# Optimization experiments

Measured on AMD Instinct MI355X. Metric: run time of the kernel, lower is better.

The kernel has to match this reference:

```python
import jax, jax.numpy as jnp
import numpy as np

A_MAX = 1.63
D_X = 0.0
E_STAR = 0.032
S_IMM = 0.14
S_INFTY = 0.049
X_H_STAR = 97.3
X_NU_STAR = 4.8
X_P_STAR = 1514.4
X_Y_STAR = 3.5
ALPHA_M = 0.9
ALPHA_M_STAR = 2.53
DELTA = 5
GAMMA_P = 2.04
NU = 4.8  # is_Garki = True
SIGMA_0 = 0.66 ** 0.5
SIGMA_I = 10.2 ** 0.5
N = 32768   # individuals
T = 365     # timesteps (max_age = T*DELTA = 1825 days)
M = 65536   # fixed infection pool (replaces dynamic tau_infidx list)


def _body_surface(age_days):
    age = jnp.minimum(age_days, 20.0 * 365.0) / 365.0
    b = 2.009715297378839e-1
    c = 1.7984405384216584e-1
    d = -2.121587990857579e-2
    e = 1.3554013908681017e-3
    f = -2.847697353524861e-5
    return b + c * age + d * age ** 2 + e * age ** 3 + f * age ** 4


def setup_inputs() -> dict:
    key = jax.random.key(0)
    k0, k1, k2, k3, k4, k5, k6 = jax.random.split(key, 7)
    EIR = jax.random.uniform(k0, (365 // DELTA,), minval=0.0, maxval=2.0)
    log_d = SIGMA_I * jax.random.normal(k1, (N,))  # log of LogNormal(0, sigma_i)
    offsets = jnp.sort(jax.random.randint(k2, (N,), 0, T * DELTA)).astype(jnp.int32)
    tau0 = jnp.floor(jax.random.uniform(k3, (M,)) * T) * DELTA          # infection start (days)
    tau_max = tau0 + jnp.exp(5.13 + 0.8 * jax.random.normal(k4, (M,)))  # infection end
    idx = jax.random.randint(k5, (M,), 0, N).astype(jnp.int32)           # host individual
    eps = jax.random.normal(k6, (T, M))                                  # parasite-density noise
    return dict(EIR=EIR, log_d=log_d, tau0=tau0, tau_max=tau_max, eps=eps,
                idx=idx, offsets=offsets)


def reference(EIR, log_d, tau0, tau_max, eps, idx, offsets):
    n = log_d.shape[0]
    Tn, Mn = eps.shape
    t_days = jnp.arange(Tn) * DELTA
    tf = t_days.astype(jnp.float32)
    eff_EIR = EIR[(t_days % 365) // DELTA] * _body_surface(tf) / A_MAX   # [T]
    D_m_t = 1.0 - ALPHA_M * jnp.exp(-(tf / 365.0 / ALPHA_M_STAR) * jnp.log(2.0))  # [T]

    # _ln_y_G time-independent pieces (per infection)
    dur = tau_max - tau0
    a = jnp.minimum(0.018 * dur, 4.4)
    c = a / (1.0 + dur / 35.0)
    b = jnp.log(a / c) / dur
    log_d_inf = log_d[idx]

    def step(carry, inp):
        X_p, X_h, X_y, _ = carry
        t_step, eps_t = inp
        t_int = t_step * DELTA
        t = t_int.astype(jnp.float32)
        act = t_int >= offsets                                  # [n] alive mask
        rel_idx = jnp.clip((t_int - offsets) // DELTA, 0, Tn - 1)
        E = jnp.where(act, eff_EIR[rel_idx], 0.0)               # [n]
        # _force_of_infection (Poisson replaced by its mean for determinism)
        S1 = S_INFTY + (1.0 - S_INFTY) / (1.0 + E / E_STAR)
        S2 = S_IMM + (1.0 - S_IMM) / (1.0 + (X_p / X_P_STAR) ** GAMMA_P)
        h_star = S1 * S2 * E
        # active infections this step
        m = (tau0 <= t) & (tau_max > t) & act[idx]              # [M]
        mf = m.astype(E.dtype)
        # _update_immunity (state BEFORE X_h update, as in original)
        sigma_y = SIGMA_0 * (1.0 + X_h / X_NU_STAR) ** -0.5     # [n]
        D_h = 1.0 / (1.0 + X_h / X_H_STAR)                      # [n]
        D_y = 1.0 / (1.0 + X_y / X_Y_STAR)                      # [M]
        Dm_i = D_m_t[rel_idx]                                   # [n]
        cnt = jax.ops.segment_sum(mf, idx, num_segments=n)      # multiplicity M
        M_inf = cnt[idx]
        ln_yG = a * jnp.exp(-b * (t - tau0)) - NU
        ln_yG = jnp.where(ln_yG <= 0.0, 1e-10, ln_yG)
        log_term = jnp.log(D_X / jnp.maximum(M_inf, 1.0) + (1.0 - D_X))
        E_ln_y = D_y * D_h[idx] * Dm_i[idx] * (log_d_inf + ln_yG) + log_term
        y = jnp.exp(E_ln_y + sigma_y[idx] * eps_t) * mf          # [M]
        Y = jax.ops.segment_sum(y, idx, num_segments=n)          # [n] total density
        X_p_new = X_p + E
        X_h_new = X_h + h_star
        X_y_new = X_y + (Y[idx] - y) * mf                        # cross-immunity
        return (X_p_new, X_h_new, X_y_new, Y), None

    init = (jnp.zeros(n), jnp.zeros(n), jnp.zeros(Mn), jnp.zeros(n))
    (X_p, X_h, X_y, Y), _ = jax.lax.scan(step, init, (jnp.arange(Tn), eps))
    return Y, X_y, X_h
```

## Files before the change

### kernel.cpp

```cpp
#include <hip/hip_runtime.h>

#define NHOST 32768
#define MINF  65536
#define TSTEPS 365
#define DELTA_ 5
#define KMAX  3
#define NGRP  4096
#define NWAVE 2048

#define C_E_STAR      0.032f
#define C_S_IMM       0.14f
#define C_S_INFTY     0.049f
#define C_X_H_STAR    97.3f
#define C_X_NU_STAR   4.8f
#define C_X_P_STAR    1514.4f
#define C_X_Y_STAR    3.5f
#define C_ALPHA_M     0.9f
#define C_ALPHA_M_ST  2.53f
#define C_GAMMA_P     2.04f
#define C_SIGMA_0     0.8124038404635961f
#define C_LN2         0.6931471805599453f


__global__ void initK(int* __restrict__ cnt, int* __restrict__ cursor) {
    int i = blockIdx.x * blockDim.x + threadIdx.x;
    if (i < NHOST) { cnt[i] = 0; cursor[i] = 0; }
}

__global__ void histK(const int* __restrict__ idx, int* __restrict__ cnt) {
    int j = blockIdx.x * blockDim.x + threadIdx.x;
    if (j < MINF) atomicAdd(&cnt[idx[j]], 1);
}

__global__ __launch_bounds__(1024) void scanK(const int* __restrict__ cnt,
                                              int* __restrict__ start) {
    __shared__ int sh[1024];
    int tid = threadIdx.x;
    int base = tid * 32;
    int s = 0;
    #pragma unroll
    for (int k = 0; k < 32; ++k) s += cnt[base + k];
    sh[tid] = s;
    __syncthreads();
    for (int o = 1; o < 1024; o <<= 1) {
        int v = 0;
        if (tid >= o) v = sh[tid - o];
        __syncthreads();
        sh[tid] += v;
        __syncthreads();
    }
    int run = sh[tid] - s;
    #pragma unroll
    for (int k = 0; k < 32; ++k) {
        start[base + k] = run;
        run += cnt[base + k];
    }
}

__global__ void scatterK(const int* __restrict__ idx,
                         const float* __restrict__ tau0,
                         const float* __restrict__ tau_max,
                         const int* __restrict__ start,
                         int* __restrict__ cursor,
                         int* __restrict__ slotJ,
                         float* __restrict__ slotT0,
                         float* __restrict__ slotT1) {
    int j = blockIdx.x * blockDim.x + threadIdx.x;
    if (j >= MINF) return;
    int h = idx[j];
    int p = start[h] + atomicAdd(&cursor[h], 1);
    slotJ[p]  = j;
    slotT0[p] = tau0[j];
    slotT1[p] = tau_max[j];
}

__global__ __launch_bounds__(512) void tableK(const float* __restrict__ EIR,
                                              float* __restrict__ sigyT,
                                              float* __restrict__ coefT,
                                              float* __restrict__ XhP) {
    __shared__ float sA[512];
    int r = threadIdx.x;
    float E = 0.0f, Dm = 0.0f;
    if (r < TSTEPS) {
        float tf  = (float)(r * DELTA_);
        float age = fminf(tf, 7300.0f) * (1.0f / 365.0f);
        float bs  = 2.009715297378839e-1f +
                    age * (1.7984405384216584e-1f +
                    age * (-2.121587990857579e-2f +
                    age * (1.3554013908681017e-3f +
                    age * (-2.847697353524861e-5f))));
        E  = EIR[r % 73] * bs * (1.0f / 1.63f);
        Dm = 1.0f - C_ALPHA_M * expf(-(tf / 365.0f / C_ALPHA_M_ST) * C_LN2);
    }
    sA[r] = E;
    __syncthreads();
    for (int o = 1; o < 512; o <<= 1) {
        float v = 0.0f;
        if (r >= o) v = sA[r - o];
        __syncthreads();
        sA[r] += v;
        __syncthreads();
    }
    float Xp = (r < TSTEPS) ? (sA[r] - E) : 0.0f;
    float S1    = C_S_INFTY + (1.0f - C_S_INFTY) / (1.0f + E * (1.0f / C_E_STAR));
    float p204  = __powf(Xp * (1.0f / C_X_P_STAR), C_GAMMA_P);
    float S2    = C_S_IMM + (1.0f - C_S_IMM) / (1.0f + p204);
    float hstar = S1 * S2 * E;
    __syncthreads();
    sA[r] = hstar;
    __syncthreads();
    for (int o = 1; o < 512; o <<= 1) {
        float v = 0.0f;
        if (r >= o) v = sA[r - o];
        __syncthreads();
        sA[r] += v;
        __syncthreads();
    }
    if (r < TSTEPS) {
        float Xh = sA[r] - hstar;
        sigyT[r] = C_SIGMA_0 * rsqrtf(1.0f + Xh * (1.0f / C_X_NU_STAR));
        coefT[r] = Dm / (1.0f + Xh * (1.0f / C_X_H_STAR));
        XhP[r]   = sA[r];
    }
}


__global__ __launch_bounds__(256) void mainK(const float* __restrict__ log_d,
                                             const int* __restrict__ offsets,
                                             const float* __restrict__ eps,
                                             const int* __restrict__ start,
                                             const int* __restrict__ cnt,
                                             const int* __restrict__ slotJ,
                                             const float* __restrict__ slotT0,
                                             const float* __restrict__ slotT1,
                                             const float* __restrict__ sigyTg,
                                             const float* __restrict__ coefTg,
                                             const float* __restrict__ XhPg,
                                             float* __restrict__ out) {
    __shared__ float sSig[TSTEPS];
    __shared__ float sCoef[TSTEPS];
    for (int k = threadIdx.x; k < TSTEPS; k += blockDim.x) {
        sSig[k]  = sigyTg[k];
        sCoef[k] = coefTg[k];
    }
    __syncthreads();

    int w    = blockIdx.x * 4 + (threadIdx.x >> 6);
    int lane = threadIdx.x & 63;
    int sub  = lane & 7;
    int hoff = lane >> 3;

    #pragma unroll 1
    for (int ph = 0; ph < 2; ++ph) {
        int g = ph ? (NGRP - 1 - w) : w;
        int h = g * 8 + hoff;

        int off = offsets[h];
        int ch  = cnt[h];
        int myCnt = (ch > sub) ? ((ch - sub + 7) >> 3) : 0;
        if (myCnt > KMAX) myCnt = KMAX;
        int base = start[h] + sub;
        float ld = log_d[h] + 1e-10f;

        int   J[KMAX];
        float T0[KMAX], T1[KMAX], Xy[KMAX], ec[KMAX];
        #pragma unroll
        for (int k = 0; k < KMAX; ++k) {
            Xy[k] = 0.0f; ec[k] = 0.0f; J[k] = 0;
            T0[k] = 1e30f; T1[k] = -1e30f;
            if (k < myCnt) {
                int p = base + 8 * k;
                J[k]  = slotJ[p];
                T0[k] = slotT0[p];
                T1[k] = slotT1[p];
            }
        }

        int tstart = (off + DELTA_ - 1) / DELTA_;
        float Ylast = 0.0f;

        if (tstart < TSTEPS) {
            float tf0 = (float)(tstart * DELTA_);
            #pragma unroll
            for (int k = 0; k < KMAX; ++k)
                if (T0[k] <= tf0 && T1[k] > tf0)
                    ec[k] = eps[(size_t)tstart * MINF + J[k]];
        }

        for (int t = tstart; t < TSTEPS; ++t) {
            float tf  = (float)(t * DELTA_);
            int   rel = t - tstart;

            float en[KMAX];
            #pragma unroll
            for (int k = 0; k < KMAX; ++k) en[k] = 0.0f;
            if (t < TSTEPS - 1) {
                float tf2 = tf + (float)DELTA_;
                #pragma unroll
                for (int k = 0; k < KMAX; ++k)
                    if (T0[k] <= tf2 && T1[k] > tf2)
                        en[k] = eps[(size_t)(t + 1) * MINF + J[k]];
            }

            float sigy = sSig[rel];
            float coef = sCoef[rel];

            float ysum = 0.0f;
            float yk[KMAX];
            bool  ak[KMAX];
            #pragma unroll
            for (int k = 0; k < KMAX; ++k) {
                bool  act = (T0[k] <= tf) & (T1[k] > tf);
                float Dy  = 1.0f / (1.0f + Xy[k] * (1.0f / C_X_Y_STAR));
                float y   = act ? __expf(Dy * coef * ld + sigy * ec[k]) : 0.0f;
                ak[k] = act; yk[k] = y; ysum += y;
            }
            float Ys = ysum + __shfl_xor(ysum, 1, 64);
            Ys += __shfl_xor(Ys, 2, 64);
            Ys += __shfl_xor(Ys, 4, 64);

            #pragma unroll
            for (int k = 0; k < KMAX; ++k)
                if (ak[k]) Xy[k] += Ys - yk[k];

            Ylast = Ys;

            #pragma unroll
            for (int k = 0; k < KMAX; ++k) ec[k] = en[k];
        }

        int iters = TSTEPS - tstart;
        if (sub == 0) {
            out[h] = Ylast;
            out[NHOST + MINF + h] = (iters > 0) ? XhPg[iters - 1] : 0.0f;
        }
        #pragma unroll
        for (int k = 0; k < KMAX; ++k)
            if (k < myCnt) out[NHOST + J[k]] = Xy[k];
    }
}


extern "C" void kernel_launch(void* const* d_in, const int* in_sizes, int n_in,
                              void* d_out, int out_size, void* d_ws, size_t ws_size,
                              hipStream_t stream) {
    const float* EIR     = (const float*)d_in[0];
    const float* log_d   = (const float*)d_in[1];
    const float* tau0    = (const float*)d_in[2];
    const float* tau_max = (const float*)d_in[3];
    const float* eps     = (const float*)d_in[4];
    const int*   idx     = (const int*)d_in[5];
    const int*   offsets = (const int*)d_in[6];
    float* out = (float*)d_out;

    char* ws = (char*)d_ws;
    int*   cnt    = (int*)ws;    ws += NHOST * sizeof(int);
    int*   start  = (int*)ws;    ws += NHOST * sizeof(int);
    int*   cursor = (int*)ws;    ws += NHOST * sizeof(int);
    int*   slotJ  = (int*)ws;    ws += MINF * sizeof(int);
    float* slotT0 = (float*)ws;  ws += MINF * sizeof(float);
    float* slotT1 = (float*)ws;  ws += MINF * sizeof(float);
    float* sigyT  = (float*)ws;  ws += TSTEPS * sizeof(float);
    float* coefT  = (float*)ws;  ws += TSTEPS * sizeof(float);
    float* XhP    = (float*)ws;  ws += TSTEPS * sizeof(float);

    initK<<<NHOST / 256, 256, 0, stream>>>(cnt, cursor);
    histK<<<MINF / 256, 256, 0, stream>>>(idx, cnt);
    scanK<<<1, 1024, 0, stream>>>(cnt, start);
    scatterK<<<MINF / 256, 256, 0, stream>>>(idx, tau0, tau_max, start, cursor,
                                             slotJ, slotT0, slotT1);
    tableK<<<1, 512, 0, stream>>>(EIR, sigyT, coefT, XhP);
    mainK<<<(NWAVE * 64) / 256, 256, 0, stream>>>(log_d, offsets, eps,
                                                  start, cnt, slotJ, slotT0, slotT1,
                                                  sigyT, coefT, XhP, out);
}
```

Baseline: 387.6 us.

## Map four lanes per host and prefetch eps two steps ahead

Each host's infections are now split across 4 lanes instead of 8, and each lane holds up to 6 infections instead of 3. The two-phase load-balancing loop over wave groups is dropped in favour of one thread group per host. The eps noise loads are software-pipelined two timesteps ahead, and the per-step table values are prefetched one step ahead. The aim is to hide global-memory latency on the dependent time loop and use fewer shuffle stages, at the cost of more registers per thread and possible imbalance between waves because offsets are sorted.

Measured after the change: 363.8 us. -6.1%, faster.

```diff
diff --git a/kernel.cpp b/kernel.cpp
--- a/kernel.cpp
+++ b/kernel.cpp
@@ -4,9 +4,7 @@
 #define MINF  65536
 #define TSTEPS 365
 #define DELTA_ 5
-#define KMAX  3
-#define NGRP  4096
-#define NWAVE 2048
+#define KMAX  6
 
 #define C_E_STAR      0.032f
 #define C_S_IMM       0.14f
@@ -137,107 +135,110 @@
                                              const float* __restrict__ coefTg,
                                              const float* __restrict__ XhPg,
                                              float* __restrict__ out) {
-    __shared__ float sSig[TSTEPS];
-    __shared__ float sCoef[TSTEPS];
+    __shared__ float sSig[TSTEPS + 1];
+    __shared__ float sCoef[TSTEPS + 1];
     for (int k = threadIdx.x; k < TSTEPS; k += blockDim.x) {
         sSig[k]  = sigyTg[k];
         sCoef[k] = coefTg[k];
     }
-    __syncthreads();
-
-    int w    = blockIdx.x * 4 + (threadIdx.x >> 6);
-    int lane = threadIdx.x & 63;
-    int sub  = lane & 7;
-    int hoff = lane >> 3;
-
-    #pragma unroll 1
-    for (int ph = 0; ph < 2; ++ph) {
-        int g = ph ? (NGRP - 1 - w) : w;
-        int h = g * 8 + hoff;
-
-        int off = offsets[h];
-        int ch  = cnt[h];
-        int myCnt = (ch > sub) ? ((ch - sub + 7) >> 3) : 0;
-        if (myCnt > KMAX) myCnt = KMAX;
-        int base = start[h] + sub;
-        float ld = log_d[h] + 1e-10f;
-
-        int   J[KMAX];
-        float T0[KMAX], T1[KMAX], Xy[KMAX], ec[KMAX];
-        #pragma unroll
-        for (int k = 0; k < KMAX; ++k) {
-            Xy[k] = 0.0f; ec[k] = 0.0f; J[k] = 0;
-            T0[k] = 1e30f; T1[k] = -1e30f;
-            if (k < myCnt) {
-                int p = base + 8 * k;
-                J[k]  = slotJ[p];
-                T0[k] = slotT0[p];
-                T1[k] = slotT1[p];
-            }
+    if (threadIdx.x == 0) { sSig[TSTEPS] = 0.0f; sCoef[TSTEPS] = 0.0f; }
+    __syncthreads();
+
+    int tid = blockIdx.x * blockDim.x + threadIdx.x;
+    int h   = tid >> 2;
+    int sub = tid & 3;
+
+    int off = offsets[h];
+    int ch  = cnt[h];
+    int myCnt = (ch > sub) ? ((ch - sub + 3) >> 2) : 0;
+    if (myCnt > KMAX) myCnt = KMAX;
+    int base = start[h] + sub;
+    float ld = log_d[h] + 1e-10f;
+
+    int   J[KMAX];
+    float T0[KMAX], T1[KMAX], Xy[KMAX], eA[KMAX], eB[KMAX];
+    #pragma unroll
+    for (int k = 0; k < KMAX; ++k) {
+        Xy[k] = 0.0f; eA[k] = 0.0f; eB[k] = 0.0f; J[k] = 0;
+        T0[k] = 1e30f; T1[k] = -1e30f;
+        if (k < myCnt) {
+            int p = base + 4 * k;
+            J[k]  = slotJ[p];
+            T0[k] = slotT0[p];
+            T1[k] = slotT1[p];
         }
-
-        int tstart = (off + DELTA_ - 1) / DELTA_;
-        float Ylast = 0.0f;
-
-        if (tstart < TSTEPS) {
-            float tf0 = (float)(tstart * DELTA_);
+    }
+
+    int tstart = (off + DELTA_ - 1) / DELTA_;
+    float Ylast = 0.0f;
+
+    if (tstart < TSTEPS) {
+        float tf0 = (float)(tstart * DELTA_);
+        #pragma unroll
+        for (int k = 0; k < KMAX; ++k)
+            if (T0[k] <= tf0 && T1[k] > tf0)
+                eA[k] = eps[(size_t)tstart * MINF + J[k]];
+    }
+    if (tstart + 1 < TSTEPS) {
+        float tf1 = (float)((tstart + 1) * DELTA_);
+        #pragma unroll
+        for (int k = 0; k < KMAX; ++k)
+            if (T0[k] <= tf1 && T1[k] > tf1)
+                eB[k] = eps[(size_t)(tstart + 1) * MINF + J[k]];
+    }
+
+    float sigy = (tstart < TSTEPS) ? sSig[0]  : 0.0f;
+    float coef = (tstart < TSTEPS) ? sCoef[0] : 0.0f;
+
+    for (int t = tstart; t < TSTEPS; ++t) {
+        float tf  = (float)(t * DELTA_);
+        int   rel = t - tstart;
+
+        float eC[KMAX];
+        #pragma unroll
+        for (int k = 0; k < KMAX; ++k) eC[k] = 0.0f;
+        if (t + 2 < TSTEPS) {
+            float tf2 = tf + 2.0f * (float)DELTA_;
             #pragma unroll
             for (int k = 0; k < KMAX; ++k)
-                if (T0[k] <= tf0 && T1[k] > tf0)
-                    ec[k] = eps[(size_t)tstart * MINF + J[k]];
+                if (T0[k] <= tf2 && T1[k] > tf2)
+                    eC[k] = eps[(size_t)(t + 2) * MINF + J[k]];
         }
-
-        for (int t = tstart; t < TSTEPS; ++t) {
-            float tf  = (float)(t * DELTA_);
-            int   rel = t - tstart;
-
-            float en[KMAX];
-            #pragma unroll
-            for (int k = 0; k < KMAX; ++k) en[k] = 0.0f;
-            if (t < TSTEPS - 1) {
-                float tf2 = tf + (float)DELTA_;
-                #pragma unroll
-                for (int k = 0; k < KMAX; ++k)
-                    if (T0[k] <= tf2 && T1[k] > tf2)
-                        en[k] = eps[(size_t)(t + 1) * MINF + J[k]];
-            }
-
-            float sigy = sSig[rel];
-            float coef = sCoef[rel];
-
-            float ysum = 0.0f;
-            float yk[KMAX];
-            bool  ak[KMAX];
-            #pragma unroll
-            for (int k = 0; k < KMAX; ++k) {
-                bool  act = (T0[k] <= tf) & (T1[k] > tf);
-                float Dy  = 1.0f / (1.0f + Xy[k] * (1.0f / C_X_Y_STAR));
-                float y   = act ? __expf(Dy * coef * ld + sigy * ec[k]) : 0.0f;
-                ak[k] = act; yk[k] = y; ysum += y;
-            }
-            float Ys = ysum + __shfl_xor(ysum, 1, 64);
-            Ys += __shfl_xor(Ys, 2, 64);
-            Ys += __shfl_xor(Ys, 4, 64);
-
-            #pragma unroll
-            for (int k = 0; k < KMAX; ++k)
-                if (ak[k]) Xy[k] += Ys - yk[k];
-
-            Ylast = Ys;
-
-            #pragma unroll
-            for (int k = 0; k < KMAX; ++k) ec[k] = en[k];
+        float sigyN = sSig[rel + 1];
+        float coefN = sCoef[rel + 1];
+
+        float ysum = 0.0f;
+        float yk[KMAX];
+        bool  ak[KMAX];
+        #pragma unroll
+        for (int k = 0; k < KMAX; ++k) {
+            bool  act = (T0[k] <= tf) & (T1[k] > tf);
+            float Dy  = 1.0f / (1.0f + Xy[k] * (1.0f / C_X_Y_STAR));
+            float y   = act ? __expf(Dy * coef * ld + sigy * eA[k]) : 0.0f;
+            ak[k] = act; yk[k] = y; ysum += y;
         }
-
-        int iters = TSTEPS - tstart;
-        if (sub == 0) {
-            out[h] = Ylast;
-            out[NHOST + MINF + h] = (iters > 0) ? XhPg[iters - 1] : 0.0f;
-        }
+        float Ys = ysum + __shfl_xor(ysum, 1, 64);
+        Ys += __shfl_xor(Ys, 2, 64);
+
         #pragma unroll
         for (int k = 0; k < KMAX; ++k)
-            if (k < myCnt) out[NHOST + J[k]] = Xy[k];
-    }
+            if (ak[k]) Xy[k] += Ys - yk[k];
+
+        Ylast = Ys;
+
+        #pragma unroll
+        for (int k = 0; k < KMAX; ++k) { eA[k] = eB[k]; eB[k] = eC[k]; }
+        sigy = sigyN; coef = coefN;
+    }
+
+    int iters = TSTEPS - tstart;
+    if (sub == 0) {
+        out[h] = Ylast;
+        out[NHOST + MINF + h] = (iters > 0) ? XhPg[iters - 1] : 0.0f;
+    }
+    #pragma unroll
+    for (int k = 0; k < KMAX; ++k)
+        if (k < myCnt) out[NHOST + J[k]] = Xy[k];
 }
 
 
@@ -270,7 +271,7 @@
     scatterK<<<MINF / 256, 256, 0, stream>>>(idx, tau0, tau_max, start, cursor,
                                              slotJ, slotT0, slotT1);
     tableK<<<1, 512, 0, stream>>>(EIR, sigyT, coefT, XhP);
-    mainK<<<(NWAVE * 64) / 256, 256, 0, stream>>>(log_d, offsets, eps,
-                                                  start, cnt, slotJ, slotT0, slotT1,
-                                                  sigyT, coefT, XhP, out);
-}
+    mainK<<<(NHOST * 4) / 256, 256, 0, stream>>>(log_d, offsets, eps,
+                                                 start, cnt, slotJ, slotT0, slotT1,
+                                                 sigyT, coefT, XhP, out);
+}
```

## Drop table kernel and remap hosts to 4 lanes with inline Xp/Xh recurrence

Applied to the files above, without the earlier changes.

Removes the separate single-block prefix-scan table kernel. mainK now builds the EIR and maturation tables in shared memory and carries the Xp and Xh recurrences per host inside the time loop. Each host now gets 4 lanes with up to 6 infections per lane instead of 8 lanes with up to 3, and the two-phase load-balance loop is replaced by a block permutation that launches 512 blocks, one host per thread group. This saves a kernel launch and table round-trip and halves the shuffle reduction. In exchange it adds per-step pow/rsqrt/div work, raises register pressure, and lengthens serial per-thread loops.

Result: slower. 492.0 us, median of 2 (+26.9%).

```diff
diff --git a/kernel.cpp b/kernel.cpp
--- a/kernel.cpp
+++ b/kernel.cpp
@@ -4,9 +4,7 @@
 #define MINF  65536
 #define TSTEPS 365
 #define DELTA_ 5
-#define KMAX  3
-#define NGRP  4096
-#define NWAVE 2048
+#define KMAX  6
 
 #define C_E_STAR      0.032f
 #define C_S_IMM       0.14f
@@ -74,58 +72,9 @@
     slotT1[p] = tau_max[j];
 }
 
-__global__ __launch_bounds__(512) void tableK(const float* __restrict__ EIR,
-                                              float* __restrict__ sigyT,
-                                              float* __restrict__ coefT,
-                                              float* __restrict__ XhP) {
-    __shared__ float sA[512];
-    int r = threadIdx.x;
-    float E = 0.0f, Dm = 0.0f;
-    if (r < TSTEPS) {
-        float tf  = (float)(r * DELTA_);
-        float age = fminf(tf, 7300.0f) * (1.0f / 365.0f);
-        float bs  = 2.009715297378839e-1f +
-                    age * (1.7984405384216584e-1f +
-                    age * (-2.121587990857579e-2f +
-                    age * (1.3554013908681017e-3f +
-                    age * (-2.847697353524861e-5f))));
-        E  = EIR[r % 73] * bs * (1.0f / 1.63f);
-        Dm = 1.0f - C_ALPHA_M * expf(-(tf / 365.0f / C_ALPHA_M_ST) * C_LN2);
-    }
-    sA[r] = E;
-    __syncthreads();
-    for (int o = 1; o < 512; o <<= 1) {
-        float v = 0.0f;
-        if (r >= o) v = sA[r - o];
-        __syncthreads();
-        sA[r] += v;
-        __syncthreads();
-    }
-    float Xp = (r < TSTEPS) ? (sA[r] - E) : 0.0f;
-    float S1    = C_S_INFTY + (1.0f - C_S_INFTY) / (1.0f + E * (1.0f / C_E_STAR));
-    float p204  = __powf(Xp * (1.0f / C_X_P_STAR), C_GAMMA_P);
-    float S2    = C_S_IMM + (1.0f - C_S_IMM) / (1.0f + p204);
-    float hstar = S1 * S2 * E;
-    __syncthreads();
-    sA[r] = hstar;
-    __syncthreads();
-    for (int o = 1; o < 512; o <<= 1) {
-        float v = 0.0f;
-        if (r >= o) v = sA[r - o];
-        __syncthreads();
-        sA[r] += v;
-        __syncthreads();
-    }
-    if (r < TSTEPS) {
-        float Xh = sA[r] - hstar;
-        sigyT[r] = C_SIGMA_0 * rsqrtf(1.0f + Xh * (1.0f / C_X_NU_STAR));
-        coefT[r] = Dm / (1.0f + Xh * (1.0f / C_X_H_STAR));
-        XhP[r]   = sA[r];
-    }
-}
-
-
-__global__ __launch_bounds__(256) void mainK(const float* __restrict__ log_d,
+
+__global__ __launch_bounds__(256) void mainK(const float* __restrict__ EIR,
+                                             const float* __restrict__ log_d,
                                              const int* __restrict__ offsets,
                                              const float* __restrict__ eps,
                                              const int* __restrict__ start,
@@ -133,111 +82,114 @@
                                              const int* __restrict__ slotJ,
                                              const float* __restrict__ slotT0,
                                              const float* __restrict__ slotT1,
-                                             const float* __restrict__ sigyTg,
-                                             const float* __restrict__ coefTg,
-                                             const float* __restrict__ XhPg,
                                              float* __restrict__ out) {
-    __shared__ float sSig[TSTEPS];
-    __shared__ float sCoef[TSTEPS];
+    __shared__ float sEff[TSTEPS];
+    __shared__ float sDm[TSTEPS];
     for (int k = threadIdx.x; k < TSTEPS; k += blockDim.x) {
-        sSig[k]  = sigyTg[k];
-        sCoef[k] = coefTg[k];
+        float tf  = (float)(k * DELTA_);
+        float age = fminf(tf, 7300.0f) * (1.0f / 365.0f);
+        float bs  = 2.009715297378839e-1f +
+                    age * (1.7984405384216584e-1f +
+                    age * (-2.121587990857579e-2f +
+                    age * (1.3554013908681017e-3f +
+                    age * (-2.847697353524861e-5f))));
+        sEff[k] = EIR[k % 73] * bs * (1.0f / 1.63f);
+        sDm[k]  = 1.0f - C_ALPHA_M * expf(-(tf / 365.0f / C_ALPHA_M_ST) * C_LN2);
     }
     __syncthreads();
 
-    int w    = blockIdx.x * 4 + (threadIdx.x >> 6);
-    int lane = threadIdx.x & 63;
-    int sub  = lane & 7;
-    int hoff = lane >> 3;
-
-    #pragma unroll 1
-    for (int ph = 0; ph < 2; ++ph) {
-        int g = ph ? (NGRP - 1 - w) : w;
-        int h = g * 8 + hoff;
-
-        int off = offsets[h];
-        int ch  = cnt[h];
-        int myCnt = (ch > sub) ? ((ch - sub + 7) >> 3) : 0;
-        if (myCnt > KMAX) myCnt = KMAX;
-        int base = start[h] + sub;
-        float ld = log_d[h] + 1e-10f;
-
-        int   J[KMAX];
-        float T0[KMAX], T1[KMAX], Xy[KMAX], ec[KMAX];
-        #pragma unroll
-        for (int k = 0; k < KMAX; ++k) {
-            Xy[k] = 0.0f; ec[k] = 0.0f; J[k] = 0;
-            T0[k] = 1e30f; T1[k] = -1e30f;
-            if (k < myCnt) {
-                int p = base + 8 * k;
-                J[k]  = slotJ[p];
-                T0[k] = slotT0[p];
-                T1[k] = slotT1[p];
-            }
+    int b  = blockIdx.x;
+    int pb = (b < 256) ? (2 * b) : (1023 - 2 * b);
+    int tid = pb * 256 + threadIdx.x;
+    int h   = tid >> 2;
+    int sub = tid & 3;
+
+    int off = offsets[h];
+    int ch  = cnt[h];
+    int myCnt = (ch > sub) ? ((ch - sub + 3) >> 2) : 0;
+    if (myCnt > KMAX) myCnt = KMAX;
+    int base = start[h] + sub;
+    float ld = log_d[h] + 1e-10f;
+
+    int   J[KMAX];
+    float T0[KMAX], T1[KMAX], Xy[KMAX], ec[KMAX];
+    #pragma unroll
+    for (int k = 0; k < KMAX; ++k) {
+        Xy[k] = 0.0f; ec[k] = 0.0f; J[k] = 0;
+        T0[k] = 1e30f; T1[k] = -1e30f;
+        if (k < myCnt) {
+            int p = base + 4 * k;
+            J[k]  = slotJ[p];
+            T0[k] = slotT0[p];
+            T1[k] = slotT1[p];
         }
-
-        int tstart = (off + DELTA_ - 1) / DELTA_;
-        float Ylast = 0.0f;
-
-        if (tstart < TSTEPS) {
-            float tf0 = (float)(tstart * DELTA_);
+    }
+
+    int tstart = (off + DELTA_ - 1) / DELTA_;
+    float Xp = 0.0f, Xh = 0.0f, Ylast = 0.0f;
+
+    if (tstart < TSTEPS) {
+        float tf0 = (float)(tstart * DELTA_);
+        #pragma unroll
+        for (int k = 0; k < KMAX; ++k)
+            if (T0[k] <= tf0 && T1[k] > tf0)
+                ec[k] = eps[(size_t)tstart * MINF + J[k]];
+    }
+
+    for (int t = tstart; t < TSTEPS; ++t) {
+        float tf  = (float)(t * DELTA_);
+        int   rel = t - tstart;
+        float E   = sEff[rel];
+        float Dm  = sDm[rel];
+
+        float en[KMAX];
+        #pragma unroll
+        for (int k = 0; k < KMAX; ++k) en[k] = 0.0f;
+        if (t < TSTEPS - 1) {
+            float tf2 = tf + (float)DELTA_;
             #pragma unroll
             for (int k = 0; k < KMAX; ++k)
-                if (T0[k] <= tf0 && T1[k] > tf0)
-                    ec[k] = eps[(size_t)tstart * MINF + J[k]];
+                if (T0[k] <= tf2 && T1[k] > tf2)
+                    en[k] = eps[(size_t)(t + 1) * MINF + J[k]];
         }
 
-        for (int t = tstart; t < TSTEPS; ++t) {
-            float tf  = (float)(t * DELTA_);
-            int   rel = t - tstart;
-
-            float en[KMAX];
-            #pragma unroll
-            for (int k = 0; k < KMAX; ++k) en[k] = 0.0f;
-            if (t < TSTEPS - 1) {
-                float tf2 = tf + (float)DELTA_;
-                #pragma unroll
-                for (int k = 0; k < KMAX; ++k)
-                    if (T0[k] <= tf2 && T1[k] > tf2)
-                        en[k] = eps[(size_t)(t + 1) * MINF + J[k]];
-            }
-
-            float sigy = sSig[rel];
-            float coef = sCoef[rel];
-
-            float ysum = 0.0f;
-            float yk[KMAX];
-            bool  ak[KMAX];
-            #pragma unroll
-            for (int k = 0; k < KMAX; ++k) {
-                bool  act = (T0[k] <= tf) & (T1[k] > tf);
-                float Dy  = 1.0f / (1.0f + Xy[k] * (1.0f / C_X_Y_STAR));
-                float y   = act ? __expf(Dy * coef * ld + sigy * ec[k]) : 0.0f;
-                ak[k] = act; yk[k] = y; ysum += y;
-            }
-            float Ys = ysum + __shfl_xor(ysum, 1, 64);
-            Ys += __shfl_xor(Ys, 2, 64);
-            Ys += __shfl_xor(Ys, 4, 64);
-
-            #pragma unroll
-            for (int k = 0; k < KMAX; ++k)
-                if (ak[k]) Xy[k] += Ys - yk[k];
-
-            Ylast = Ys;
-
-            #pragma unroll
-            for (int k = 0; k < KMAX; ++k) ec[k] = en[k];
+        float S1    = C_S_INFTY + (1.0f - C_S_INFTY) / (1.0f + E * (1.0f / C_E_STAR));
+        float p204  = __powf(Xp * (1.0f / C_X_P_STAR), C_GAMMA_P);
+        float S2    = C_S_IMM + (1.0f - C_S_IMM) / (1.0f + p204);
+        float hstar = S1 * S2 * E;
+        float sigy  = C_SIGMA_0 * rsqrtf(1.0f + Xh * (1.0f / C_X_NU_STAR));
+        float coef  = Dm / (1.0f + Xh * (1.0f / C_X_H_STAR));
+
+        float ysum = 0.0f;
+        float yk[KMAX];
+        bool  ak[KMAX];
+        #pragma unroll
+        for (int k = 0; k < KMAX; ++k) {
+            bool  act = (T0[k] <= tf) & (T1[k] > tf);
+            float Dy  = 1.0f / (1.0f + Xy[k] * (1.0f / C_X_Y_STAR));
+            float y   = act ? __expf(Dy * coef * ld + sigy * ec[k]) : 0.0f;
+            ak[k] = act; yk[k] = y; ysum += y;
         }
-
-        int iters = TSTEPS - tstart;
-        if (sub == 0) {
-            out[h] = Ylast;
-            out[NHOST + MINF + h] = (iters > 0) ? XhPg[iters - 1] : 0.0f;
-        }
+        float Ys = ysum + __shfl_xor(ysum, 1, 64);
+        Ys += __shfl_xor(Ys, 2, 64);
+
         #pragma unroll
         for (int k = 0; k < KMAX; ++k)
-            if (k < myCnt) out[NHOST + J[k]] = Xy[k];
-    }
+            if (ak[k]) Xy[k] += Ys - yk[k];
+
+        Xp += E; Xh += hstar; Ylast = Ys;
+
+        #pragma unroll
+        for (int k = 0; k < KMAX; ++k) ec[k] = en[k];
+    }
+
+    if (sub == 0) {
+        out[h] = Ylast;
+        out[NHOST + MINF + h] = Xh;
+    }
+    #pragma unroll
+    for (int k = 0; k < KMAX; ++k)
+        if (k < myCnt) out[NHOST + J[k]] = Xy[k];
 }
 
 
@@ -260,17 +212,13 @@
     int*   slotJ  = (int*)ws;    ws += MINF * sizeof(int);
     float* slotT0 = (float*)ws;  ws += MINF * sizeof(float);
     float* slotT1 = (float*)ws;  ws += MINF * sizeof(float);
-    float* sigyT  = (float*)ws;  ws += TSTEPS * sizeof(float);
-    float* coefT  = (float*)ws;  ws += TSTEPS * sizeof(float);
-    float* XhP    = (float*)ws;  ws += TSTEPS * sizeof(float);
 
     initK<<<NHOST / 256, 256, 0, stream>>>(cnt, cursor);
     histK<<<MINF / 256, 256, 0, stream>>>(idx, cnt);
     scanK<<<1, 1024, 0, stream>>>(cnt, start);
     scatterK<<<MINF / 256, 256, 0, stream>>>(idx, tau0, tau_max, start, cursor,
                                              slotJ, slotT0, slotT1);
-    tableK<<<1, 512, 0, stream>>>(EIR, sigyT, coefT, XhP);
-    mainK<<<(NWAVE * 64) / 256, 256, 0, stream>>>(log_d, offsets, eps,
-                                                  start, cnt, slotJ, slotT0, slotT1,
-                                                  sigyT, coefT, XhP, out);
-}
+    mainK<<<(NHOST * 4) / 256, 256, 0, stream>>>(EIR, log_d, offsets, eps,
+                                                 start, cnt, slotJ, slotT0, slotT1,
+                                                 out);
+}
```
